# Kernel optimization log

Hardware: AMD Instinct MI355X
Metric: run time of the kernel (lower is better)

## Reference

```python
import jax, jax.numpy as jnp
import numpy as np

B, T, C = 64, 200, 53
EMB, HID, AH, OUT = 64, 128, 128, 2
C2 = C * C
D1 = round(0.05 * C2)   # 140
D2 = round(0.5 * C2)    # 1404
BN_EPS = 1e-5


def setup_inputs() -> dict:
    key = jax.random.key(0)
    ks = jax.random.split(key, 32)
    def rn(k, shape, s=0.1):
        return (jax.random.normal(k, shape) * s).astype(jnp.float32)
    return {
        "x": rn(ks[0], (B, T, C), 1.0),
        # single shared Linear(1, EMB) embedding
        "emb_w": rn(ks[1], (EMB,)), "emb_b": rn(ks[2], (EMB,)),
        # GRU cell (weights stored [in, 3*HID], gate order r,z,n like torch)
        "w_ih": rn(ks[3], (EMB, 3 * HID)), "w_hh": rn(ks[4], (HID, 3 * HID)),
        "b_ih": rn(ks[5], (3 * HID,)), "b_hh": rn(ks[6], (3 * HID,)),
        # self-attention projections
        "q_w": rn(ks[7], (HID, AH)), "q_b": rn(ks[8], (AH,)),
        "k_w": rn(ks[9], (HID, AH)), "k_b": rn(ks[10], (AH,)),
        "v_w": rn(ks[11], (HID, HID)), "v_b": rn(ks[12], (HID,)),
        "gate_b": rn(ks[13], (C, C), 1.0),  # Gate.bias = randn(C, C)
        # gta_embed + BatchNorm1d + gta_attend
        "ge_w": rn(ks[14], (C2, D1)), "ge_b": rn(ks[15], (D1,)),
        "bn_g": jnp.ones((D1,), jnp.float32), "bn_b": jnp.zeros((D1,), jnp.float32),
        "ga_w1": rn(ks[16], (D1, D2)), "ga_b1": rn(ks[17], (D2,)),
        "ga_w2": rn(ks[18], (D2, 1)), "ga_b2": rn(ks[19], (1,)),
        # classifier MLP
        "c_w1": rn(ks[20], (C2, C2 // 2)), "c_b1": rn(ks[21], (C2 // 2,)),
        "c_w2": rn(ks[22], (C2 // 2, C2 // 4)), "c_b2": rn(ks[23], (C2 // 4,)),
        "c_w3": rn(ks[24], (C2 // 4, OUT)), "c_b3": rn(ks[25], (OUT,)),
    }


def _forward(x, emb_w, emb_b, w_ih, w_hh, b_ih, b_hh, q_w, q_b, k_w, k_b,
             v_w, v_b, gate_b, ge_w, ge_b, bn_g, bn_b, ga_w1, ga_b1, ga_w2,
             ga_b2, c_w1, c_b1, c_w2, c_b2, c_w3, c_b3):
    # Linear(1, EMB) applied per scalar: [B,T,C] -> [B,C,T,EMB]
    e = x.transpose(0, 2, 1)[..., None] * emb_w + emb_b
    xs = jnp.moveaxis(e, 2, 0)  # [T, B, C, EMB]

    def step(h, x_t):  # h: [B,C,HID], x_t: [B,C,EMB]
        gi = x_t @ w_ih + b_ih
        gh = h @ w_hh + b_hh
        i_r, i_z, i_n = jnp.split(gi, 3, axis=-1)
        h_r, h_z, h_n = jnp.split(gh, 3, axis=-1)
        r = jax.nn.sigmoid(i_r + h_r)
        z = jax.nn.sigmoid(i_z + h_z)
        n = jnp.tanh(i_n + r * h_n)
        h_new = (1 - z) * n + z * h
        # SVD-normalized self-attention across components
        q = h_new @ q_w + q_b
        k = h_new @ k_w + k_b
        v = h_new @ v_w + v_b
        scores = jnp.tanh(jnp.einsum('bif,bjf->bij', q, k))  # use_tan='before'
        sv = jnp.linalg.svd(scores, compute_uv=False)         # [B,C]
        ev = jax.lax.stop_gradient(jnp.max(jnp.abs(sv), axis=1))[:, None, None]
        scores = scores / ev
        attn = scores * jax.nn.sigmoid(jnp.abs(scores) + gate_b)  # Gate
        h_out = jnp.einsum('bij,bjf->bif', attn, v)
        return h_out, attn

    h0 = jnp.zeros((B, C, HID), x.dtype)
    _, attns = jax.lax.scan(step, h0, xs)      # [T,B,C,C]
    align = jnp.moveaxis(attns, 0, 1)          # [B,T,C,C]

    # gta_attention over time axis
    ai = align.reshape(B, T, C2)
    xr = (ai * ai.mean(axis=1, keepdims=True)).reshape(B * T, C2)
    xe = xr @ ge_w + ge_b
    mu = xe.mean(axis=0)
    var = xe.var(axis=0)  # biased, matches torch BN training-mode normalization
    xn = jax.nn.relu((xe - mu) / jnp.sqrt(var + BN_EPS) * bn_g + bn_b)
    a = jax.nn.relu(xn @ ga_w1 + ga_b1) @ ga_w2 + ga_b2  # [B*T,1]
    w = jax.nn.softmax(a.reshape(B, T), axis=1)
    dnc = (ai * w[..., None]).sum(axis=1)      # [B, C2]

    # classifier (Dropout1d is identity at inference)
    h1 = jax.nn.relu(dnc @ c_w1 + c_b1)
    h2 = jax.nn.relu(h1 @ c_w2 + c_b2)
    logits = h2 @ c_w3 + c_b3
    return logits, dnc.reshape(B, C, C), align


def reference(x, emb_w, emb_b, w_ih, w_hh, b_ih, b_hh, q_w, q_b, k_w, k_b,
              v_w, v_b, gate_b, ge_w, ge_b, bn_g, bn_b, ga_w1, ga_b1, ga_w2,
              ga_b2, c_w1, c_b1, c_w2, c_b2, c_w3, c_b3):
    return _forward(x, emb_w, emb_b, w_ih, w_hh, b_ih, b_hh, q_w, q_b, k_w,
                    k_b, v_w, v_b, gate_b, ge_w, ge_b, bn_g, bn_b, ga_w1,
                    ga_b1, ga_w2, ga_b2, c_w1, c_b1, c_w2, c_b2, c_w3, c_b3)
```

## Files before the change

### kernel.cpp

```cpp
#include <hip/hip_runtime.h>

#define NT 1024

__device__ __forceinline__ float fast_sigmoid(float x) { return 1.f/(1.f + __expf(-x)); }
__device__ __forceinline__ float fast_tanh(float x) {
  float t = __expf(-2.f*fabsf(x));
  float y = (1.f - t)/(1.f + t);
  return copysignf(y, x);
}
__device__ __forceinline__ void acc4(float& a, float4 u, float4 v) {
  a = fmaf(u.x, v.x, a); a = fmaf(u.y, v.y, a); a = fmaf(u.z, v.z, a); a = fmaf(u.w, v.w, a);
}
#define FMA4(A_, S_, V_) do { (A_).x = fmaf((S_),(V_).x,(A_).x); (A_).y = fmaf((S_),(V_).y,(A_).y); \
                              (A_).z = fmaf((S_),(V_).z,(A_).z); (A_).w = fmaf((S_),(V_).w,(A_).w); } while(0)

struct alignas(16) SmemScan {
  float h[56][132];
  float hh[56][132];
  float v[56][132];
  union {
    float z[53][132];
    float G[2][56][60];
  } ab;
  float S[56][60];
  float G0[56][60];
  float u384[384], v00[384];
  float gb[2812];
  float xt[56];
  float pv[56], y1[56], y2[56];
  int   gmax[9];
  float sc_ev;
};

__global__ void prep_wp1(const float* __restrict__ w_hh, const float* __restrict__ b_hh,
                         float* __restrict__ Wp1) {
  int idx = blockIdx.x*256 + threadIdx.x;
  if (idx >= 3*33*128*4) return;
  int j = idx & 3;
  int f = (idx >> 2) & 127;
  int qg = idx >> 9;
  int q = qg % 33;
  int g = qg / 33;
  int k = 4*q + j;
  int col = g*128 + f;
  float v = 0.f;
  if (k < 128) v = w_hh[k*384 + col];
  else if (k == 128) v = b_hh[col];
  Wp1[idx] = v;
}

__global__ void prep_wp2(const float* __restrict__ q_w, const float* __restrict__ q_b,
                         const float* __restrict__ k_w, const float* __restrict__ k_b,
                         const float* __restrict__ v_w, const float* __restrict__ v_b,
                         float* __restrict__ Wp2) {
  int idx = blockIdx.x*256 + threadIdx.x;
  if (idx >= 33924) return;
  float val = 0.f;
  if (idx < 33792) {
    int j = idx & 3;
    int f = (idx >> 2) & 127;
    int qp = idx >> 9;
    int q = qp % 33;
    int p = qp / 33;
    int u = 2*f + p;
    int k = 4*q + j;
    if (u < 129) {
      if (k <= 128) {
        const float* qa = (k < 128) ? (q_w + k*128) : q_b;
        const float* kb = (u < 128) ? (k_w + u*128) : k_b;
        float s = 0.f;
        for (int d = 0; d < 128; ++d) s = fmaf(qa[d], kb[d], s);
        val = s;
      }
    } else {
      int f2 = u - 129;
      if (k < 128) val = v_w[k*128 + f2];
      else if (k == 128) val = v_b[f2];
    }
  } else {
    int c = idx - 33792;
    if (c < 128) val = v_w[c*128 + 127];
    else if (c == 128) val = v_b[127];
  }
  Wp2[idx] = val;
}

__global__ void __launch_bounds__(1024, 4)
scan_kernel(const float* __restrict__ x, const float* __restrict__ emb_w,
            const float* __restrict__ emb_b, const float* __restrict__ w_ih,
            const float* __restrict__ b_ih, const float* __restrict__ Wp1,
            const float* __restrict__ Wp2, const float* __restrict__ gate_b,
            float* __restrict__ out_align)
{
  extern __shared__ char smem_raw[];
  SmemScan& sm = *reinterpret_cast<SmemScan*>(smem_raw);
  const int b = blockIdx.x;
  const int tid = threadIdx.x;
  const int wv = tid >> 6;
  const int lane = tid & 63;

  for (int j = tid; j < 384; j += NT) {
    float su = 0.f, sv = 0.f;
    for (int m = 0; m < 64; ++m) {
      float w = w_ih[m*384 + j];
      su = fmaf(emb_w[m], w, su);
      sv = fmaf(emb_b[m], w, sv);
    }
    sm.u384[j] = su;
    sm.v00[j]  = sv + b_ih[j];
  }
  for (int idx = tid; idx < 56*132; idx += NT) {
    int r = idx/132, c = idx - r*132;
    float hv = (c == 128 && r < 53) ? 1.f : 0.f;
    sm.h[r][c] = hv; sm.hh[r][c] = hv; sm.v[r][c] = 0.f;
  }
  for (int idx = tid; idx < 53*132; idx += NT) (&sm.ab.z[0][0])[idx] = 0.f;
  for (int idx = tid; idx < 56*60; idx += NT) {
    int r = idx/60, c = idx - r*60;
    sm.S[r][c] = 0.f; sm.G0[r][c] = 0.f;
  }
  for (int idx = tid; idx < 2809; idx += NT) sm.gb[idx] = gate_b[idx];
  __syncthreads();

  const int f  = tid & 127;
  const int c0 = tid >> 7;
  int  cix[7]; bool cok[7];
  #pragma unroll
  for (int i = 0; i < 7; ++i) { int cc = c0 + 8*i; cok[i] = (cc < 53); cix[i] = cok[i] ? cc : 52; }

  const float* pw1 = Wp1 + (size_t)f*4;
  const float* pw2 = Wp2 + (size_t)f*4;
  const float* W256 = Wp2 + 33792;
  const int colA = 2*f, colB = colA + 1;

  float xreg = 0.f;
  if (tid < 53) xreg = x[(b*200)*53 + tid];

  for (int t = 0; t < 200; ++t) {
    if (tid < 53) sm.xt[tid] = xreg;
    __syncthreads();
    if (tid < 53 && t < 199) xreg = x[(b*200 + t + 1)*53 + tid];

    float a0[7], a1[7], a2[7];
    #pragma unroll
    for (int i = 0; i < 7; ++i) { a0[i] = 0.f; a1[i] = 0.f; a2[i] = 0.f; }
    {
      float4 w0 = *(const float4*)(pw1);
      float4 w1 = *(const float4*)(pw1 + 16896);
      float4 w2 = *(const float4*)(pw1 + 33792);
      for (int q = 0; q < 33; ++q) {
        float4 n0 = w0, n1 = w1, n2 = w2;
        if (q < 32) {
          const float* p = pw1 + (q+1)*512;
          n0 = *(const float4*)(p);
          n1 = *(const float4*)(p + 16896);
          n2 = *(const float4*)(p + 33792);
        }
        #pragma unroll
        for (int i = 0; i < 7; ++i) {
          float4 hv = *(const float4*)&sm.h[cix[i]][4*q];
          acc4(a0[i], hv, w0); acc4(a1[i], hv, w1); acc4(a2[i], hv, w2);
        }
        w0 = n0; w1 = n1; w2 = n2;
      }
    }
    {
      float uf0 = sm.u384[f], uf1 = sm.u384[128+f], uf2 = sm.u384[256+f];
      float v0f0 = sm.v00[f], v0f1 = sm.v00[128+f], v0f2 = sm.v00[256+f];
      #pragma unroll
      for (int i = 0; i < 7; ++i) {
        float xs = sm.xt[cix[i]];
        float r = fast_sigmoid(fmaf(xs, uf0, v0f0) + a0[i]);
        float z = fast_sigmoid(fmaf(xs, uf1, v0f1) + a1[i]);
        float n = fast_tanh(fmaf(xs, uf2, v0f2) + fmaf(r, a2[i], 0.f));
        float hn = (1.f - z)*n + z*sm.h[cix[i]][f];
        if (cok[i]) sm.hh[cix[i]][f] = hn;
      }
    }
    __syncthreads();

    {
      float aA[7], aB[7];
      #pragma unroll
      for (int i = 0; i < 7; ++i) { aA[i] = 0.f; aB[i] = 0.f; }
      float4 wa = *(const float4*)(pw2);
      float4 wb = *(const float4*)(pw2 + 16896);
      for (int q = 0; q < 33; ++q) {
        float4 na = wa, nb = wb;
        if (q < 32) {
          const float* p = pw2 + (q+1)*512;
          na = *(const float4*)(p);
          nb = *(const float4*)(p + 16896);
        }
        #pragma unroll
        for (int i = 0; i < 7; ++i) {
          float4 hv = *(const float4*)&sm.hh[cix[i]][4*q];
          acc4(aA[i], hv, wa); acc4(aB[i], hv, wb);
        }
        wa = na; wb = nb;
      }
      #pragma unroll
      for (int i = 0; i < 7; ++i) if (cok[i]) {
        int c = cix[i];
        if (colA < 129) sm.ab.z[c][colA] = aA[i]; else sm.v[c][colA-129] = aA[i];
        if (colB < 129) sm.ab.z[c][colB] = aB[i]; else sm.v[c][colB-129] = aB[i];
      }
      if (tid < 53) {
        float s = 0.f;
        for (int q = 0; q < 33; ++q) {
          float4 wv4 = *(const float4*)(W256 + 4*q);
          float4 hv = *(const float4*)&sm.hh[tid][4*q];
          acc4(s, hv, wv4);
        }
        sm.v[tid][127] = s;
      }
    }
    __syncthreads();

    if (tid < 9) sm.gmax[tid] = 0;
    if (wv < 14 && lane < 53) {
      const int i = lane, j0 = 4*wv;
      float4 acc; acc.x = acc.y = acc.z = acc.w = 0.f;
      for (int q = 0; q < 33; ++q) {
        float4 zr = *(const float4*)&sm.ab.z[i][4*q];
        float4 h0 = *(const float4*)&sm.hh[j0  ][4*q];
        float4 h1 = *(const float4*)&sm.hh[j0+1][4*q];
        float4 h2 = *(const float4*)&sm.hh[j0+2][4*q];
        float4 h3 = *(const float4*)&sm.hh[j0+3][4*q];
        acc4(acc.x, zr, h0); acc4(acc.y, zr, h1); acc4(acc.z, zr, h2); acc4(acc.w, zr, h3);
      }
      sm.S[i][j0  ] = fast_tanh(acc.x);
      sm.S[i][j0+1] = fast_tanh(acc.y);
      sm.S[i][j0+2] = fast_tanh(acc.z);
      sm.S[i][j0+3] = fast_tanh(acc.w);
    }
    __syncthreads();

    {
      float mx = 0.f;
      if (wv < 14 && lane < 53) {
        const int i = lane, j0 = 4*wv;
        float4 acc; acc.x = acc.y = acc.z = acc.w = 0.f;
        for (int q = 0; q < 14; ++q) {
          float4 sr = *(const float4*)&sm.S[i][4*q];
          float4 s0 = *(const float4*)&sm.S[j0  ][4*q];
          float4 s1 = *(const float4*)&sm.S[j0+1][4*q];
          float4 s2 = *(const float4*)&sm.S[j0+2][4*q];
          float4 s3 = *(const float4*)&sm.S[j0+3][4*q];
          acc4(acc.x, sr, s0); acc4(acc.y, sr, s1); acc4(acc.z, sr, s2); acc4(acc.w, sr, s3);
        }
        sm.G0[i][j0] = acc.x; sm.G0[i][j0+1] = acc.y;
        sm.G0[i][j0+2] = acc.z; sm.G0[i][j0+3] = acc.w;
        mx = fmaxf(fmaxf(fabsf(acc.x), fabsf(acc.y)), fmaxf(fabsf(acc.z), fabsf(acc.w)));
      }
      if (wv < 14) {
        for (int off = 32; off; off >>= 1) mx = fmaxf(mx, __shfl_down(mx, off));
        if (lane == 0) atomicMax(&sm.gmax[0], __float_as_int(mx));
      } else {
        float* GAB = &sm.ab.G[0][0][0];
        for (int l = tid - 896; l < 180; l += 128) {
          GAB[3180 + l] = 0.f;
          GAB[6540 + l] = 0.f;
        }
      }
    }
    __syncthreads();

    float (*pa)[60] = sm.G0;
    float (*pc)[60] = sm.ab.G[0];
    for (int k = 0; k < 7; ++k) {
      float mx = 0.f;
      if (wv < 14 && lane < 53) {
        float s = 1.f/fmaxf(__int_as_float(sm.gmax[k]), 1e-20f);
        const int i = lane, j0 = 4*wv;
        float4 acc; acc.x = acc.y = acc.z = acc.w = 0.f;
        for (int q = 0; q < 14; ++q) {
          float4 ar = *(const float4*)&pa[i][4*q];
          float4 b0 = *(const float4*)&pa[j0  ][4*q];
          float4 b1 = *(const float4*)&pa[j0+1][4*q];
          float4 b2 = *(const float4*)&pa[j0+2][4*q];
          float4 b3 = *(const float4*)&pa[j0+3][4*q];
          acc4(acc.x, ar, b0); acc4(acc.y, ar, b1); acc4(acc.z, ar, b2); acc4(acc.w, ar, b3);
        }
        float s2 = s*s;
        acc.x *= s2; acc.y *= s2; acc.z *= s2; acc.w *= s2;
        pc[i][j0] = acc.x; pc[i][j0+1] = acc.y; pc[i][j0+2] = acc.z; pc[i][j0+3] = acc.w;
        mx = fmaxf(fmaxf(fabsf(acc.x), fabsf(acc.y)), fmaxf(fabsf(acc.z), fabsf(acc.w)));
      }
      if (wv < 14) {
        for (int off = 32; off; off >>= 1) mx = fmaxf(mx, __shfl_down(mx, off));
        if (lane == 0) atomicMax(&sm.gmax[k+1], __float_as_int(mx));
      }
      __syncthreads();
      float (*tn)[60] = pc;
      pc = (pc == sm.ab.G[0]) ? sm.ab.G[1] : sm.ab.G[0];
      pa = tn;
    }

    if (wv == 0) {
      if (lane < 53) {
        float s = 0.f;
        for (int j = 0; j < 53; ++j) {
          float ph = 0.618034f*(float)(j + 1);
          float rj = 0.75f + 0.5f*(ph - floorf(ph));
          s = fmaf(pa[j][lane], rj, s);
        }
        sm.pv[lane] = s;
      }
      __builtin_amdgcn_sched_barrier(0);
      if (lane < 53) {
        float s = 0.f;
        for (int j = 0; j < 53; ++j) s = fmaf(sm.G0[j][lane], sm.pv[j], s);
        sm.y1[lane] = s;
      }
      __builtin_amdgcn_sched_barrier(0);
      if (lane < 53) {
        float s = 0.f;
        for (int j = 0; j < 53; ++j) s = fmaf(sm.G0[j][lane], sm.y1[j], s);
        sm.y2[lane] = s;
      }
      __builtin_amdgcn_sched_barrier(0);
      float y3v = 0.f, y2v = 0.f;
      if (lane < 53) {
        float s = 0.f;
        for (int j = 0; j < 53; ++j) s = fmaf(sm.G0[j][lane], sm.y2[j], s);
        y3v = s; y2v = sm.y2[lane];
      }
      float num = y2v*y3v, den = y2v*y2v;
      for (int off = 32; off; off >>= 1) { num += __shfl_down(num, off); den += __shfl_down(den, off); }
      if (lane == 0) sm.sc_ev = sqrtf(num/fmaxf(den, 1e-30f));
    }
    __syncthreads();

    {
      float inv = 1.f/sm.sc_ev;
      const size_t abase = ((size_t)b*200 + (size_t)t)*2809;
      for (int idx = tid; idx < 2809; idx += NT) {
        int i = idx/53, j = idx - i*53;
        float s = sm.S[i][j]*inv;
        float a = s*fast_sigmoid(fabsf(s) + sm.gb[idx]);
        sm.S[i][j] = a;
        __builtin_nontemporal_store(a, &out_align[abase + idx]);
      }
    }
    __syncthreads();

    {
      const int f0 = (tid & 31)*4;
      const int io = tid >> 5;
      const int i1 = io + 32;
      const bool has1 = (i1 < 53);
      float4 acc0, acc1;
      acc0.x = acc0.y = acc0.z = acc0.w = 0.f;
      acc1 = acc0;
      for (int q = 0; q < 14; ++q) {
        float4 s0 = *(const float4*)&sm.S[io][4*q];
        float4 s1 = *(const float4*)&sm.S[has1 ? i1 : 0][4*q];
        int j = 4*q;
        float4 v0 = *(const float4*)&sm.v[j  ][f0];
        float4 v1 = *(const float4*)&sm.v[j+1][f0];
        float4 v2 = *(const float4*)&sm.v[j+2][f0];
        float4 v3 = *(const float4*)&sm.v[j+3][f0];
        FMA4(acc0, s0.x, v0); FMA4(acc0, s0.y, v1); FMA4(acc0, s0.z, v2); FMA4(acc0, s0.w, v3);
        FMA4(acc1, s1.x, v0); FMA4(acc1, s1.y, v1); FMA4(acc1, s1.z, v2); FMA4(acc1, s1.w, v3);
      }
      *(float4*)&sm.h[io][f0] = acc0;
      if (has1) *(float4*)&sm.h[i1][f0] = acc1;
    }
  }
}


__global__ void mean_kernel(const float* __restrict__ align, float* __restrict__ m) {
  int idx = blockIdx.x*256 + threadIdx.x;
  if (idx >= 64*2809) return;
  int b = idx/2809, c = idx - b*2809;
  const float* p = align + (size_t)b*200*2809 + c;
  float s = 0.f;
  for (int t = 0; t < 200; ++t) s += p[(size_t)t*2809];
  m[idx] = s*(1.f/200.f);
}

__global__ void __launch_bounds__(256) xe_kernel(const float* __restrict__ align,
    const float* __restrict__ mai, const float* __restrict__ ge_w,
    const float* __restrict__ ge_b, float* __restrict__ xe) {
  __shared__ float sai[8][64];
  __shared__ float sw[64][140];
  const int tid = threadIdx.x;
  const int r0 = blockIdx.x*8;
  float4 acc0, acc1;
  acc0.x = acc0.y = acc0.z = acc0.w = 0.f;
  acc1 = acc0;
  const bool active = tid < 140;
  int rr0 = 0, cc0 = 0;
  if (active) { rr0 = (tid/35)*2; cc0 = (tid - 35*(tid/35))*4; }
  for (int k0 = 0; k0 < 2809; k0 += 64) {
    for (int l = tid; l < 512; l += 256) {
      int rr = l >> 6, kk = l & 63, k = k0 + kk;
      int r = r0 + rr;
      int bb = r/200;
      sai[rr][kk] = (k < 2809) ? align[(size_t)r*2809 + k]*mai[bb*2809 + k] : 0.f;
    }
    for (int l = tid; l < 64*140; l += 256) {
      int kk = l/140, cc = l - kk*140, k = k0 + kk;
      sw[kk][cc] = (k < 2809) ? ge_w[k*140 + cc] : 0.f;
    }
    __syncthreads();
    if (active) {
      for (int kk = 0; kk < 64; ++kk) {
        float a0 = sai[rr0][kk], a1 = sai[rr0+1][kk];
        float4 wv = *(const float4*)&sw[kk][cc0];
        FMA4(acc0, a0, wv); FMA4(acc1, a1, wv);
      }
    }
    __syncthreads();
  }
  if (active) {
    float4 gb = *(const float4*)&ge_b[cc0];
    acc0.x += gb.x; acc0.y += gb.y; acc0.z += gb.z; acc0.w += gb.w;
    acc1.x += gb.x; acc1.y += gb.y; acc1.z += gb.z; acc1.w += gb.w;
    *(float4*)&xe[(r0 + rr0)*140 + cc0]   = acc0;
    *(float4*)&xe[(r0 + rr0 + 1)*140 + cc0] = acc1;
  }
}

__global__ void bn_stats_kernel(const float* __restrict__ xe, float* __restrict__ mu,
                                float* __restrict__ var) {
  const int c = blockIdx.x, tid = threadIdx.x;
  double s = 0.0, sq = 0.0;
  for (int r = tid; r < 12800; r += 256) {
    double v = (double)xe[r*140 + c];
    s += v; sq += v*v;
  }
  for (int off = 32; off; off >>= 1) { s += __shfl_down(s, off); sq += __shfl_down(sq, off); }
  __shared__ double rs[4], rq[4];
  if ((tid & 63) == 0) { rs[tid >> 6] = s; rq[tid >> 6] = sq; }
  __syncthreads();
  if (tid == 0) {
    double S = rs[0]+rs[1]+rs[2]+rs[3], Q = rq[0]+rq[1]+rq[2]+rq[3];
    double m = S/12800.0;
    double v = Q/12800.0 - m*m;
    mu[c] = (float)m;
    var[c] = (float)fmax(v, 0.0);
  }
}

__global__ void __launch_bounds__(256) a_kernel(const float* __restrict__ xe,
    const float* __restrict__ mu, const float* __restrict__ var,
    const float* __restrict__ bn_g, const float* __restrict__ bn_b,
    const float* __restrict__ ga_w1, const float* __restrict__ ga_b1,
    const float* __restrict__ ga_w2, const float* __restrict__ ga_b2,
    float* __restrict__ a_out) {
  __shared__ float sxn[16][140];
  __shared__ float rsum[16];
  const int tid = threadIdx.x;
  const int r0 = blockIdx.x*16;
  for (int l = tid; l < 16*140; l += 256) {
    int rr = l/140, cc = l - rr*140;
    float v = xe[(r0 + rr)*140 + cc];
    float xn = (v - mu[cc])*rsqrtf(var[cc] + 1e-5f)*bn_g[cc] + bn_b[cc];
    sxn[rr][cc] = fmaxf(xn, 0.f);
  }
  if (tid < 16) rsum[tid] = 0.f;
  __syncthreads();
  float asum[16];
  #pragma unroll
  for (int r = 0; r < 16; ++r) asum[r] = 0.f;
  for (int j = tid; j < 1404; j += 256) {
    float acc[16];
    #pragma unroll
    for (int r = 0; r < 16; ++r) acc[r] = 0.f;
    for (int k = 0; k < 140; ++k) {
      float wv = ga_w1[k*1404 + j];
      #pragma unroll
      for (int r = 0; r < 16; ++r) acc[r] += sxn[r][k]*wv;
    }
    float b1 = ga_b1[j], w2 = ga_w2[j];
    #pragma unroll
    for (int r = 0; r < 16; ++r) asum[r] += fmaxf(acc[r] + b1, 0.f)*w2;
  }
  #pragma unroll
  for (int r = 0; r < 16; ++r) atomicAdd(&rsum[r], asum[r]);
  __syncthreads();
  if (tid < 16) a_out[r0 + tid] = rsum[tid] + ga_b2[0];
}

__global__ void softmax_kernel(const float* __restrict__ a, float* __restrict__ w) {
  const int b = blockIdx.x, tid = threadIdx.x;
  float mx = -1e30f;
  for (int t = tid; t < 200; t += 64) mx = fmaxf(mx, a[b*200 + t]);
  for (int off = 32; off; off >>= 1) mx = fmaxf(mx, __shfl_down(mx, off));
  mx = __shfl(mx, 0);
  float s = 0.f;
  for (int t = tid; t < 200; t += 64) { float e = __expf(a[b*200 + t] - mx); w[b*200 + t] = e; s += e; }
  for (int off = 32; off; off >>= 1) s += __shfl_down(s, off);
  s = __shfl(s, 0);
  float inv = 1.f/s;
  for (int t = tid; t < 200; t += 64) w[b*200 + t] *= inv;
}

__global__ void dnc_kernel(const float* __restrict__ align, const float* __restrict__ w,
                           float* __restrict__ dnc) {
  int idx = blockIdx.x*256 + threadIdx.x;
  if (idx >= 64*2809) return;
  int b = idx/2809, c = idx - b*2809;
  const float* p = align + (size_t)b*200*2809 + c;
  const float* pw = w + b*200;
  float s = 0.f;
  for (int t = 0; t < 200; ++t) s += p[(size_t)t*2809]*pw[t];
  dnc[idx] = s;
}

__global__ void fc_relu_kernel(const float* __restrict__ in, const float* __restrict__ wgt,
    const float* __restrict__ bias, float* __restrict__ out, int rows, int K, int N) {
  int idx = blockIdx.x*256 + threadIdx.x;
  if (idx >= rows*N) return;
  int r = idx/N, j = idx - r*N;
  const float* pi = in + (size_t)r*K;
  float s = 0.f;
  for (int k = 0; k < K; ++k) s += pi[k]*wgt[k*N + j];
  out[idx] = fmaxf(s + bias[j], 0.f);
}

__global__ void fc_kernel(const float* __restrict__ in, const float* __restrict__ wgt,
    const float* __restrict__ bias, float* __restrict__ out, int rows, int K, int N) {
  int idx = blockIdx.x*256 + threadIdx.x;
  if (idx >= rows*N) return;
  int r = idx/N, j = idx - r*N;
  const float* pi = in + (size_t)r*K;
  float s = 0.f;
  for (int k = 0; k < K; ++k) s += pi[k]*wgt[k*N + j];
  out[idx] = s + bias[j];
}

extern "C" void kernel_launch(void* const* d_in, const int* in_sizes, int n_in,
                              void* d_out, int out_size, void* d_ws, size_t ws_size,
                              hipStream_t stream) {
  (void)in_sizes; (void)n_in; (void)out_size; (void)ws_size;
  const float* x      = (const float*)d_in[0];
  const float* emb_w  = (const float*)d_in[1];
  const float* emb_b  = (const float*)d_in[2];
  const float* w_ih   = (const float*)d_in[3];
  const float* w_hh   = (const float*)d_in[4];
  const float* b_ih   = (const float*)d_in[5];
  const float* b_hh   = (const float*)d_in[6];
  const float* q_w    = (const float*)d_in[7];
  const float* q_b    = (const float*)d_in[8];
  const float* k_w    = (const float*)d_in[9];
  const float* k_b    = (const float*)d_in[10];
  const float* v_w    = (const float*)d_in[11];
  const float* v_b    = (const float*)d_in[12];
  const float* gate_b = (const float*)d_in[13];
  const float* ge_w   = (const float*)d_in[14];
  const float* ge_b   = (const float*)d_in[15];
  const float* bn_g   = (const float*)d_in[16];
  const float* bn_b   = (const float*)d_in[17];
  const float* ga_w1  = (const float*)d_in[18];
  const float* ga_b1  = (const float*)d_in[19];
  const float* ga_w2  = (const float*)d_in[20];
  const float* ga_b2  = (const float*)d_in[21];
  const float* c_w1   = (const float*)d_in[22];
  const float* c_b1   = (const float*)d_in[23];
  const float* c_w2   = (const float*)d_in[24];
  const float* c_b2   = (const float*)d_in[25];
  const float* c_w3   = (const float*)d_in[26];
  const float* c_b3   = (const float*)d_in[27];

  float* out = (float*)d_out;
  float* out_logits = out;
  float* out_dnc    = out + 128;
  float* out_align  = out + 128 + 64*2809;

  float* ws    = (float*)d_ws;
  float* w_Wp1 = ws;
  float* w_Wp2 = w_Wp1 + 50688;
  float* w_m   = w_Wp2 + 33924;
  float* w_xe  = w_m + 179776;
  float* w_mu  = w_xe + 1792000;
  float* w_var = w_mu + 140;
  float* w_a   = w_var + 140;
  float* w_w   = w_a + 12800;
  float* w_h1  = w_w + 12800;
  float* w_h2  = w_h1 + 89856;

  hipLaunchKernelGGL(prep_wp1, dim3((50688 + 255)/256), dim3(256), 0, stream, w_hh, b_hh, w_Wp1);
  hipLaunchKernelGGL(prep_wp2, dim3((33924 + 255)/256), dim3(256), 0, stream,
                     q_w, q_b, k_w, k_b, v_w, v_b, w_Wp2);

  const size_t shmem = sizeof(SmemScan);
  (void)hipFuncSetAttribute(reinterpret_cast<const void*>(scan_kernel),
                            hipFuncAttributeMaxDynamicSharedMemorySize, (int)shmem);

  hipLaunchKernelGGL(scan_kernel, dim3(64), dim3(1024), shmem, stream,
                     x, emb_w, emb_b, w_ih, b_ih, w_Wp1, w_Wp2, gate_b, out_align);

  hipLaunchKernelGGL(mean_kernel, dim3(703), dim3(256), 0, stream, out_align, w_m);
  hipLaunchKernelGGL(xe_kernel, dim3(1600), dim3(256), 0, stream, out_align, w_m, ge_w, ge_b, w_xe);
  hipLaunchKernelGGL(bn_stats_kernel, dim3(140), dim3(256), 0, stream, w_xe, w_mu, w_var);
  hipLaunchKernelGGL(a_kernel, dim3(800), dim3(256), 0, stream,
                     w_xe, w_mu, w_var, bn_g, bn_b, ga_w1, ga_b1, ga_w2, ga_b2, w_a);
  hipLaunchKernelGGL(softmax_kernel, dim3(64), dim3(64), 0, stream, w_a, w_w);
  hipLaunchKernelGGL(dnc_kernel, dim3(703), dim3(256), 0, stream, out_align, w_w, out_dnc);
  hipLaunchKernelGGL(fc_relu_kernel, dim3(351), dim3(256), 0, stream, out_dnc, c_w1, c_b1, w_h1, 64, 2809, 1404);
  hipLaunchKernelGGL(fc_relu_kernel, dim3(176), dim3(256), 0, stream, w_h1, c_w2, c_b2, w_h2, 64, 1404, 702);
  hipLaunchKernelGGL(fc_kernel, dim3(1), dim3(128), 0, stream, w_h2, c_w3, c_b3, out_logits, 64, 702, 2);
}
```

Measured before the change: 32.04 ms.

## Run repeated Gram-matrix squaring on bf16 MFMA instead of fp32 FMA

The seven repeated squarings of the 53x53 Gram matrix (a power-iteration style norm estimate) now use 16x16x32 bf16 MFMA instructions. The matrix is kept in a single zero-padded 64x80 bf16 shared buffer and updated in place, which replaces the fp32 ping-pong buffers. The per-step fp32 FMA loops were limited to 14 waves, while all 16 waves now each compute one 16x16 tile. This trades precision for speed, since bf16 rounding of the repeatedly squared matrix may perturb the estimate that feeds later normalization.

Measured after the change: 29.79 ms. 7.0% less time.

```diff
diff --git a/kernel.cpp b/kernel.cpp
--- a/kernel.cpp
+++ b/kernel.cpp
@@ -1,6 +1,9 @@
 #include <hip/hip_runtime.h>
 
 #define NT 1024
+
+typedef __attribute__((ext_vector_type(8))) short bf16x8;
+typedef __attribute__((ext_vector_type(4))) float f32x4;
 
 __device__ __forceinline__ float fast_sigmoid(float x) { return 1.f/(1.f + __expf(-x)); }
 __device__ __forceinline__ float fast_tanh(float x) {
@@ -10,6 +13,11 @@
 }
 __device__ __forceinline__ void acc4(float& a, float4 u, float4 v) {
   a = fmaf(u.x, v.x, a); a = fmaf(u.y, v.y, a); a = fmaf(u.z, v.z, a); a = fmaf(u.w, v.w, a);
+}
+__device__ __forceinline__ unsigned short bf16r(float x) {
+  unsigned int u = __float_as_uint(x);
+  u += 0x7FFFu + ((u >> 16) & 1u);
+  return (unsigned short)(u >> 16);
 }
 #define FMA4(A_, S_, V_) do { (A_).x = fmaf((S_),(V_).x,(A_).x); (A_).y = fmaf((S_),(V_).y,(A_).y); \
                               (A_).z = fmaf((S_),(V_).z,(A_).z); (A_).w = fmaf((S_),(V_).w,(A_).w); } while(0)
@@ -20,7 +28,7 @@
   float v[56][132];
   union {
     float z[53][132];
-    float G[2][56][60];
+    unsigned short Abf[64][80];
   } ab;
   float S[56][60];
   float G0[56][60];
@@ -133,6 +141,10 @@
   const float* W256 = Wp2 + 33792;
   const int colA = 2*f, colB = colA + 1;
 
+  const int tr = wv >> 2, tc = wv & 3;
+  const int frow = lane & 15;
+  const int fkb  = (lane >> 4) * 16;
+
   float xreg = 0.f;
   if (tid < 53) xreg = x[(b*200)*53 + tid];
 
@@ -251,50 +263,54 @@
         }
         sm.G0[i][j0] = acc.x; sm.G0[i][j0+1] = acc.y;
         sm.G0[i][j0+2] = acc.z; sm.G0[i][j0+3] = acc.w;
+        ushort4 pk;
+        pk.x = bf16r(acc.x); pk.y = bf16r(acc.y);
+        pk.z = bf16r(acc.z); pk.w = bf16r(acc.w);
+        *(ushort4*)&sm.ab.Abf[i][j0] = pk;
         mx = fmaxf(fmaxf(fabsf(acc.x), fabsf(acc.y)), fmaxf(fabsf(acc.z), fabsf(acc.w)));
       }
       if (wv < 14) {
         for (int off = 32; off; off >>= 1) mx = fmaxf(mx, __shfl_down(mx, off));
         if (lane == 0) atomicMax(&sm.gmax[0], __float_as_int(mx));
       } else {
-        float* GAB = &sm.ab.G[0][0][0];
-        for (int l = tid - 896; l < 180; l += 128) {
-          GAB[3180 + l] = 0.f;
-          GAB[6540 + l] = 0.f;
-        }
-      }
-    }
-    __syncthreads();
-
-    float (*pa)[60] = sm.G0;
-    float (*pc)[60] = sm.ab.G[0];
+        uint4 zz = make_uint4(0u, 0u, 0u, 0u);
+        for (int l = tid - 896; l < 141; l += 128) {
+          if (l < 64) {
+            *(uint4*)&sm.ab.Abf[l][56] = zz;
+          } else {
+            int m = l - 64;
+            int r = 53 + m/7, cc = (m - 7*(m/7))*8;
+            *(uint4*)&sm.ab.Abf[r][cc] = zz;
+          }
+        }
+      }
+    }
+    __syncthreads();
+
     for (int k = 0; k < 7; ++k) {
-      float mx = 0.f;
-      if (wv < 14 && lane < 53) {
-        float s = 1.f/fmaxf(__int_as_float(sm.gmax[k]), 1e-20f);
-        const int i = lane, j0 = 4*wv;
-        float4 acc; acc.x = acc.y = acc.z = acc.w = 0.f;
-        for (int q = 0; q < 14; ++q) {
-          float4 ar = *(const float4*)&pa[i][4*q];
-          float4 b0 = *(const float4*)&pa[j0  ][4*q];
-          float4 b1 = *(const float4*)&pa[j0+1][4*q];
-          float4 b2 = *(const float4*)&pa[j0+2][4*q];
-          float4 b3 = *(const float4*)&pa[j0+3][4*q];
-          acc4(acc.x, ar, b0); acc4(acc.y, ar, b1); acc4(acc.z, ar, b2); acc4(acc.w, ar, b3);
-        }
-        float s2 = s*s;
-        acc.x *= s2; acc.y *= s2; acc.z *= s2; acc.w *= s2;
-        pc[i][j0] = acc.x; pc[i][j0+1] = acc.y; pc[i][j0+2] = acc.z; pc[i][j0+3] = acc.w;
-        mx = fmaxf(fmaxf(fabsf(acc.x), fabsf(acc.y)), fmaxf(fabsf(acc.z), fabsf(acc.w)));
-      }
-      if (wv < 14) {
-        for (int off = 32; off; off >>= 1) mx = fmaxf(mx, __shfl_down(mx, off));
-        if (lane == 0) atomicMax(&sm.gmax[k+1], __float_as_int(mx));
-      }
+      const unsigned short* rA = &sm.ab.Abf[16*tr + frow][0];
+      const unsigned short* rB = &sm.ab.Abf[16*tc + frow][0];
+      bf16x8 fa0 = *(const bf16x8*)((const char*)rA + fkb);
+      bf16x8 fb0 = *(const bf16x8*)((const char*)rB + fkb);
+      bf16x8 fa1 = *(const bf16x8*)((const char*)rA + 64 + fkb);
+      bf16x8 fb1 = *(const bf16x8*)((const char*)rB + 64 + fkb);
+      float s = 1.f/fmaxf(__int_as_float(sm.gmax[k]), 1e-20f);
       __syncthreads();
-      float (*tn)[60] = pc;
-      pc = (pc == sm.ab.G[0]) ? sm.ab.G[1] : sm.ab.G[0];
-      pa = tn;
+      f32x4 acc = {0.f, 0.f, 0.f, 0.f};
+      acc = __builtin_amdgcn_mfma_f32_16x16x32_bf16(fa0, fb0, acc, 0, 0, 0);
+      acc = __builtin_amdgcn_mfma_f32_16x16x32_bf16(fa1, fb1, acc, 0, 0, 0);
+      float s2 = s*s;
+      float c0v = acc[0]*s2, c1v = acc[1]*s2, c2v = acc[2]*s2, c3v = acc[3]*s2;
+      float mx = fmaxf(fmaxf(fabsf(c0v), fabsf(c1v)), fmaxf(fabsf(c2v), fabsf(c3v)));
+      for (int off = 32; off; off >>= 1) mx = fmaxf(mx, __shfl_down(mx, off));
+      if (lane == 0) atomicMax(&sm.gmax[k+1], __float_as_int(mx));
+      const int colb = 16*tc + (lane & 15);
+      const int rowb = 16*tr + ((lane >> 4) << 2);
+      sm.ab.Abf[rowb  ][colb] = bf16r(c0v);
+      sm.ab.Abf[rowb+1][colb] = bf16r(c1v);
+      sm.ab.Abf[rowb+2][colb] = bf16r(c2v);
+      sm.ab.Abf[rowb+3][colb] = bf16r(c3v);
+      __syncthreads();
     }
 
     if (wv == 0) {
@@ -303,7 +319,8 @@
         for (int j = 0; j < 53; ++j) {
           float ph = 0.618034f*(float)(j + 1);
           float rj = 0.75f + 0.5f*(ph - floorf(ph));
-          s = fmaf(pa[j][lane], rj, s);
+          float av = __uint_as_float((unsigned)sm.ab.Abf[j][lane] << 16);
+          s = fmaf(av, rj, s);
         }
         sm.pv[lane] = s;
       }
```
